# Optimization experiments

Hardware: AMD Instinct MI355X
Metric: run time of the kernel (lower is better)

## Reference

```python
import jax, jax.numpy as jnp
import numpy as np

N_NODES = 10000
N_EDGES = 80000
IN_DIM = 1024
HID = 4096
OUT = 256


def sage_conv(x, src, dst, W_l, b_l, W_r, num_nodes):
    # mean aggregation of source-node features onto target nodes
    msg = x[src]                                            # [E, D] gather
    agg = jax.ops.segment_sum(msg, dst, num_segments=num_nodes)   # [N, D]
    cnt = jax.ops.segment_sum(jnp.ones((src.shape[0],), x.dtype), dst,
                              num_segments=num_nodes)       # [N]
    mean = agg / jnp.clip(cnt, 1.0)[:, None]                # isolated nodes -> 0
    # lin_l(mean) + lin_r(x); lin_r has no bias in PyG SAGEConv
    return mean @ W_l.T + b_l + x @ W_r.T


def setup_inputs() -> dict:
    key = jax.random.key(0)
    ks = jax.random.split(key, 6)
    x = jax.random.normal(ks[0], (N_NODES, IN_DIM), dtype=jnp.float32)
    edge_index = jax.random.randint(ks[1], (2, N_EDGES), 0, N_NODES, dtype=jnp.int32)
    s1 = 1.0 / np.sqrt(IN_DIM)
    s2 = 1.0 / np.sqrt(HID)
    W1_l = jax.random.normal(ks[2], (HID, IN_DIM), dtype=jnp.float32) * s1
    b1_l = jnp.zeros((HID,), jnp.float32)
    W1_r = jax.random.normal(ks[3], (HID, IN_DIM), dtype=jnp.float32) * s1
    W2_l = jax.random.normal(ks[4], (OUT, HID), dtype=jnp.float32) * s2
    b2_l = jnp.zeros((OUT,), jnp.float32)
    W2_r = jax.random.normal(ks[5], (OUT, HID), dtype=jnp.float32) * s2
    return {"x": x, "edge_index": edge_index, "W1_l": W1_l, "b1_l": b1_l,
            "W1_r": W1_r, "W2_l": W2_l, "b2_l": b2_l, "W2_r": W2_r}


def reference(x, edge_index, W1_l, b1_l, W1_r, W2_l, b2_l, W2_r):
    src, dst = edge_index[0], edge_index[1]
    h = sage_conv(x, src, dst, W1_l, b1_l, W1_r, N_NODES)   # [N, 4096]
    h = jax.nn.relu(h)
    # dropout is identity in eval mode
    out = sage_conv(h, src, dst, W2_l, b2_l, W2_r, N_NODES)  # [N, 256]
    return jax.nn.log_softmax(out, axis=1)
```

## Files before the change

### kernel.cpp

```cpp
#include <hip/hip_runtime.h>
#include <cstdint>
#include <cstddef>

#define DEVINL __device__ __forceinline__

typedef __bf16 bf16x8 __attribute__((ext_vector_type(8)));
typedef float f32x4 __attribute__((ext_vector_type(4)));

static constexpr int NN = 10000;
static constexpr int NE = 80000;
static constexpr int IN_DIM = 1024;
static constexpr int HID = 4096;
static constexpr int OUTD = 256;
static constexpr int M_PAD = 10112;

DEVINL unsigned short f2bf(float f) {
  unsigned int u = __builtin_bit_cast(unsigned int, f);
  u += 0x7fffu + ((u >> 16) & 1u);
  return (unsigned short)(u >> 16);
}
DEVINL float bf2f(unsigned short h) {
  unsigned int u = ((unsigned int)h) << 16;
  return __builtin_bit_cast(float, u);
}

DEVINL void ld_lds16(const void* g, void* l) {
  __builtin_amdgcn_global_load_lds(
      (const __attribute__((address_space(1))) unsigned int*)g,
      (__attribute__((address_space(3))) unsigned int*)l, 16, 0, 0);
}

static constexpr int PREP_B1 = 8192;
static constexpr int PREP_B2 = PREP_B1 + 2048;
static constexpr int PREP_B3 = PREP_B2 + 10000;
static constexpr int PREP_NB = PREP_B3 + 313;

__global__ __launch_bounds__(256) void prep_kernel(
    const float* __restrict__ W1l, const float* __restrict__ W1r,
    const float* __restrict__ W2l, const float* __restrict__ W2r,
    const float* __restrict__ x, const int* __restrict__ dst,
    unsigned short* __restrict__ w1cat, unsigned short* __restrict__ w2cat,
    unsigned short* __restrict__ x_bf, int* __restrict__ deg) {
  int b = blockIdx.x;
  int t = threadIdx.x;
  if (b < PREP_B1) {
    int g = b * 256 + t;
    int n = g >> 9;
    int kg = g & 511;
    const float* s = (kg < 256) ? (W1l + (size_t)n * 1024 + kg * 4)
                                : (W1r + (size_t)n * 1024 + (kg - 256) * 4);
    float4 v = *(const float4*)s;
    ushort4 p = {f2bf(v.x), f2bf(v.y), f2bf(v.z), f2bf(v.w)};
    ((ushort4*)w1cat)[g] = p;
  } else if (b < PREP_B2) {
    int g = (b - PREP_B1) * 256 + t;
    int n = g >> 10;
    int kg = g & 1023;
    const float* s = (n < 256) ? (W2l + (size_t)n * 4096 + kg * 4)
                               : (W2r + (size_t)(n - 256) * 4096 + kg * 4);
    float4 v = *(const float4*)s;
    ushort4 p = {f2bf(v.x), f2bf(v.y), f2bf(v.z), f2bf(v.w)};
    ((ushort4*)w2cat)[g] = p;
  } else if (b < PREP_B3) {
    int g = (b - PREP_B2) * 256 + t;
    int i = g >> 8;
    int kg = g & 255;
    float4 v = ((const float4*)(x + (size_t)i * IN_DIM))[kg];
    ushort4 p = {f2bf(v.x), f2bf(v.y), f2bf(v.z), f2bf(v.w)};
    ((ushort4*)(x_bf + (size_t)i * IN_DIM))[kg] = p;
  } else {
    int e = (b - PREP_B3) * 256 + t;
    if (e < NE) atomicAdd(&deg[dst[e]], 1);
  }
}

__global__ __launch_bounds__(256) void scan_kernel(const int* __restrict__ deg,
                                                   int* __restrict__ offs) {
  __shared__ int part[256];
  constexpr int NPT = 40;
  int t = threadIdx.x;
  int base = t * NPT;
  int s = 0;
  for (int j = 0; j < NPT; ++j) {
    int n = base + j;
    s += (n < NN) ? deg[n] : 0;
  }
  part[t] = s;
  __syncthreads();
  for (int o = 1; o < 256; o <<= 1) {
    int v = (t >= o) ? part[t - o] : 0;
    __syncthreads();
    part[t] += v;
    __syncthreads();
  }
  int pre = (t > 0) ? part[t - 1] : 0;
  for (int j = 0; j < NPT; ++j) {
    int n = base + j;
    if (n < NN) {
      offs[n] = pre;
      pre += deg[n];
    }
  }
  if (t == 255) offs[NN] = part[255];
}

__global__ void bin_kernel(const int* __restrict__ src, const int* __restrict__ dst,
                           const int* __restrict__ offs, int* __restrict__ fill,
                           int* __restrict__ csr) {
  int e = blockIdx.x * 256 + threadIdx.x;
  if (e < NE) {
    int d = dst[e];
    int p = atomicAdd(&fill[d], 1);
    csr[offs[d] + p] = src[e];
  }
}

__global__ __launch_bounds__(256) void gather1_kernel(const unsigned short* __restrict__ x_bf,
                                                      const int* __restrict__ offs,
                                                      const int* __restrict__ csr,
                                                      unsigned short* __restrict__ A1) {
  int i = blockIdx.x;
  int t = threadIdx.x;
  int beg = offs[i], end = offs[i + 1];
  float4 acc = {0.f, 0.f, 0.f, 0.f};
  for (int j = beg; j < end; ++j) {
    int s = __builtin_amdgcn_readfirstlane(csr[j]);
    ushort4 u = ((const ushort4*)(x_bf + (size_t)s * IN_DIM))[t];
    acc.x += bf2f(u.x); acc.y += bf2f(u.y); acc.z += bf2f(u.z); acc.w += bf2f(u.w);
  }
  float inv = 1.0f / (float)max(end - beg, 1);
  ushort4 ub = ((const ushort4*)(x_bf + (size_t)i * IN_DIM))[t];
  ushort4 pa = {f2bf(acc.x * inv), f2bf(acc.y * inv), f2bf(acc.z * inv), f2bf(acc.w * inv)};
  unsigned short* row = A1 + (size_t)i * 2048;
  ((ushort4*)row)[t] = pa;
  ((ushort4*)(row + 1024))[t] = ub;
}

template <int BM, int K, int N, int NUMM, int NUMN, int GM, int EPI>
__global__ __launch_bounds__(256) void gemm_kernel(const unsigned short* __restrict__ A,
                                                   const unsigned short* __restrict__ Bt,
                                                   const float* __restrict__ bias,
                                                   void* __restrict__ C0out,
                                                   void* __restrict__ C1out) {
  constexpr int BN = 128;
  constexpr int MI = BM / 32;
  constexpr int NI = 4;
  constexpr int SA = BM / 64;
  constexpr int SB = BN / 64;
  __shared__ unsigned short Asm[BM * 32];
  __shared__ unsigned short Bsm[BN * 32];

  constexpr int NPG = GM * NUMN;
  const int pid = blockIdx.x;
  const int gid = pid / NPG;
  const int first_m = gid * GM;
  const int sz = (NUMM - first_m < GM) ? (NUMM - first_m) : GM;
  const int local = pid % NPG;
  const int pm = first_m + local % sz;
  const int pn = local / sz;

  const int tid = threadIdx.x;
  const int lane = tid & 63;
  const int wave = tid >> 6;
  const int quad = lane >> 4;
  const int l16 = lane & 15;
  const int wm = (wave & 1) * (BM / 2);
  const int wn = (wave >> 1) * 64;
  const long tm0 = (long)pm * BM;
  const long tn0 = (long)pn * BN;

  f32x4 acc[MI][NI];
#pragma unroll
  for (int i = 0; i < MI; ++i)
#pragma unroll
    for (int j = 0; j < NI; ++j) acc[i][j] = (f32x4){0.f, 0.f, 0.f, 0.f};

  const unsigned short* aSrc[SA];
  unsigned short* aDst[SA];
  const unsigned short* bSrc[SB];
  unsigned short* bDst[SB];
#pragma unroll
  for (int s = 0; s < SA; ++s) {
    int c = s * 256 + wave * 64 + lane;
    int r = c >> 2;
    int g = (c & 3) ^ ((r >> 1) & 3);
    aSrc[s] = A + (size_t)(tm0 + r) * K + g * 8;
    aDst[s] = Asm + s * 2048 + wave * 512;
  }
#pragma unroll
  for (int s = 0; s < SB; ++s) {
    int c = s * 256 + wave * 64 + lane;
    int r = c >> 2;
    int g = (c & 3) ^ ((r >> 1) & 3);
    bSrc[s] = Bt + (size_t)(tn0 + r) * K + g * 8;
    bDst[s] = Bsm + s * 2048 + wave * 512;
  }

  const int srd = quad ^ ((l16 >> 1) & 3);

  for (int k0 = 0; k0 < K; k0 += 32) {
#pragma unroll
    for (int s = 0; s < SA; ++s) ld_lds16(aSrc[s] + k0, aDst[s]);
#pragma unroll
    for (int s = 0; s < SB; ++s) ld_lds16(bSrc[s] + k0, bDst[s]);
    __syncthreads();

    bf16x8 af[MI], bv[NI];
#pragma unroll
    for (int i = 0; i < MI; ++i) {
      int ra = wm + i * 16 + l16;
      af[i] = *(const bf16x8*)(Asm + ra * 32 + srd * 8);
    }
#pragma unroll
    for (int j = 0; j < NI; ++j) {
      int rb = wn + j * 16 + l16;
      bv[j] = *(const bf16x8*)(Bsm + rb * 32 + srd * 8);
    }
#pragma unroll
    for (int i = 0; i < MI; ++i)
#pragma unroll
      for (int j = 0; j < NI; ++j)
        acc[i][j] = __builtin_amdgcn_mfma_f32_16x16x32_bf16(af[i], bv[j], acc[i][j], 0, 0, 0);
    __syncthreads();
  }

  if (EPI == 1) {
    unsigned short* C = (unsigned short*)C0out;
#pragma unroll
    for (int i = 0; i < MI; ++i) {
      long m0 = tm0 + wm + i * 16 + quad * 4;
#pragma unroll
      for (int j = 0; j < NI; ++j) {
        int n = (int)tn0 + wn + j * 16 + l16;
        float bvs = bias[n];
#pragma unroll
        for (int r = 0; r < 4; ++r) {
          float v = acc[i][j][r] + bvs;
          v = fmaxf(v, 0.0f);
          C[(size_t)(m0 + r) * N + n] = f2bf(v);
        }
      }
    }
  } else {
    unsigned short* PL = (unsigned short*)C0out;
    float* PR = (float*)C1out;
#pragma unroll
    for (int i = 0; i < MI; ++i) {
      long m0 = tm0 + wm + i * 16 + quad * 4;
#pragma unroll
      for (int j = 0; j < NI; ++j) {
        int n = (int)tn0 + wn + j * 16 + l16;
        if (n < 256) {
#pragma unroll
          for (int r = 0; r < 4; ++r) PL[(size_t)(m0 + r) * 256 + n] = f2bf(acc[i][j][r]);
        } else {
#pragma unroll
          for (int r = 0; r < 4; ++r) PR[(size_t)(m0 + r) * 256 + (n - 256)] = acc[i][j][r];
        }
      }
    }
  }
}

__global__ __launch_bounds__(128) void gather2_final_kernel(const unsigned short* __restrict__ pl,
                                                            const float* __restrict__ pr,
                                                            const int* __restrict__ offs,
                                                            const int* __restrict__ csr,
                                                            const float* __restrict__ b2,
                                                            float* __restrict__ out) {
  int i = blockIdx.x;
  int t = threadIdx.x;
  int beg = offs[i], end = offs[i + 1];
  float a0 = 0.f, a1 = 0.f;
  for (int j = beg; j < end; ++j) {
    int s = __builtin_amdgcn_readfirstlane(csr[j]);
    unsigned int u = ((const unsigned int*)(pl + (size_t)s * 256))[t];
    a0 += bf2f((unsigned short)(u & 0xffffu));
    a1 += bf2f((unsigned short)(u >> 16));
  }
  float inv = 1.0f / (float)max(end - beg, 1);
  float2 bv = ((const float2*)b2)[t];
  float2 pv = ((const float2*)(pr + (size_t)i * 256))[t];
  float v0 = a0 * inv + bv.x + pv.x;
  float v1 = a1 * inv + bv.y + pv.y;

  __shared__ float sm[2], ss[2];
  int w = t >> 6;
  float m = fmaxf(v0, v1);
#pragma unroll
  for (int o = 32; o > 0; o >>= 1) m = fmaxf(m, __shfl_xor(m, o, 64));
  if ((t & 63) == 0) sm[w] = m;
  __syncthreads();
  m = fmaxf(sm[0], sm[1]);

  float s = __expf(v0 - m) + __expf(v1 - m);
#pragma unroll
  for (int o = 32; o > 0; o >>= 1) s += __shfl_xor(s, o, 64);
  if ((t & 63) == 0) ss[w] = s;
  __syncthreads();
  float ls = logf(ss[0] + ss[1]);

  float2 o2 = {v0 - m - ls, v1 - m - ls};
  ((float2*)(out + (size_t)i * OUTD))[t] = o2;
}

static constexpr size_t OFF_A1 = 0;
static constexpr size_t OFF_W1 = OFF_A1 + (size_t)M_PAD * 2048 * 2;
static constexpr size_t OFF_HB = OFF_W1 + (size_t)HID * 2048 * 2;
static constexpr size_t OFF_W2 = OFF_HB + (size_t)M_PAD * HID * 2;
static constexpr size_t OFF_XBF = OFF_W2 - (size_t)NN * IN_DIM * 2;
static constexpr size_t OFF_DEG = OFF_W2 + (size_t)512 * HID * 2;
static constexpr size_t OFF_OFFS = OFF_DEG + (size_t)NN * 4;
static constexpr size_t OFF_FILL = OFF_OFFS + (size_t)(NN + 4) * 4;
static constexpr size_t OFF_CSR = OFF_FILL + (size_t)NN * 4;
static constexpr size_t OFF_PL = OFF_A1;
static constexpr size_t OFF_PR = OFF_PL + (size_t)M_PAD * 256 * 2;

extern "C" void kernel_launch(void* const* d_in, const int* in_sizes, int n_in,
                              void* d_out, int out_size, void* d_ws, size_t ws_size,
                              hipStream_t stream) {
  const float* x = (const float*)d_in[0];
  const int* ei = (const int*)d_in[1];
  const int* src = ei;
  const int* dst = ei + NE;
  const float* W1_l = (const float*)d_in[2];
  const float* b1_l = (const float*)d_in[3];
  const float* W1_r = (const float*)d_in[4];
  const float* W2_l = (const float*)d_in[5];
  const float* b2_l = (const float*)d_in[6];
  const float* W2_r = (const float*)d_in[7];
  float* out = (float*)d_out;

  char* ws = (char*)d_ws;
  unsigned short* A1 = (unsigned short*)(ws + OFF_A1);
  unsigned short* w1cat = (unsigned short*)(ws + OFF_W1);
  unsigned short* h_b = (unsigned short*)(ws + OFF_HB);
  unsigned short* x_bf = (unsigned short*)(ws + OFF_XBF);
  unsigned short* w2cat = (unsigned short*)(ws + OFF_W2);
  int* deg = (int*)(ws + OFF_DEG);
  int* offs = (int*)(ws + OFF_OFFS);
  int* fill = (int*)(ws + OFF_FILL);
  int* csr = (int*)(ws + OFF_CSR);
  unsigned short* pl = (unsigned short*)(ws + OFF_PL);
  float* pr = (float*)(ws + OFF_PR);

  hipMemsetAsync(deg, 0, (size_t)NN * 4, stream);
  hipMemsetAsync(fill, 0, (size_t)NN * 4, stream);
  hipMemsetAsync(A1 + (size_t)NN * 2048, 0, (size_t)(M_PAD - NN) * 2048 * 2, stream);

  prep_kernel<<<PREP_NB, 256, 0, stream>>>(W1_l, W1_r, W2_l, W2_r, x, dst,
                                           w1cat, w2cat, x_bf, deg);
  scan_kernel<<<1, 256, 0, stream>>>(deg, offs);
  bin_kernel<<<(NE + 255) / 256, 256, 0, stream>>>(src, dst, offs, fill, csr);

  gather1_kernel<<<NN, 256, 0, stream>>>(x_bf, offs, csr, A1);

  gemm_kernel<128, 2048, 4096, 79, 32, 32, 1>
      <<<79 * 32, 256, 0, stream>>>(A1, w1cat, b1_l, h_b, nullptr);
  gemm_kernel<64, 4096, 512, 158, 4, 64, 2>
      <<<158 * 4, 256, 0, stream>>>(h_b, w2cat, nullptr, pl, pr);

  gather2_final_kernel<<<NN, 128, 0, stream>>>(pl, pr, offs, csr, b2_l, out);
}
```

Before: 483.9 us.

## Double GEMM K-tile to 64 and fold CSR fill counter into scan

```diff
diff --git a/kernel.cpp b/kernel.cpp
--- a/kernel.cpp
+++ b/kernel.cpp
@@ -75,7 +75,8 @@
 }
 
 __global__ __launch_bounds__(256) void scan_kernel(const int* __restrict__ deg,
-                                                   int* __restrict__ offs) {
+                                                   int* __restrict__ offs,
+                                                   int* __restrict__ cur) {
   __shared__ int part[256];
   constexpr int NPT = 40;
   int t = threadIdx.x;
@@ -98,6 +99,7 @@
     int n = base + j;
     if (n < NN) {
       offs[n] = pre;
+      cur[n] = pre;
       pre += deg[n];
     }
   }
@@ -105,13 +107,11 @@
 }
 
 __global__ void bin_kernel(const int* __restrict__ src, const int* __restrict__ dst,
-                           const int* __restrict__ offs, int* __restrict__ fill,
-                           int* __restrict__ csr) {
+                           int* __restrict__ cur, int* __restrict__ csr) {
   int e = blockIdx.x * 256 + threadIdx.x;
   if (e < NE) {
-    int d = dst[e];
-    int p = atomicAdd(&fill[d], 1);
-    csr[offs[d] + p] = src[e];
+    int p = atomicAdd(&cur[dst[e]], 1);
+    csr[p] = src[e];
   }
 }
 
@@ -145,10 +145,10 @@
   constexpr int BN = 128;
   constexpr int MI = BM / 32;
   constexpr int NI = 4;
-  constexpr int SA = BM / 64;
-  constexpr int SB = BN / 64;
-  __shared__ unsigned short Asm[BM * 32];
-  __shared__ unsigned short Bsm[BN * 32];
+  constexpr int SA = BM / 32;
+  constexpr int SB = BN / 32;
+  __shared__ unsigned short Asm[BM * 64];
+  __shared__ unsigned short Bsm[BN * 64];
 
   constexpr int NPG = GM * NUMN;
   const int pid = blockIdx.x;
@@ -182,45 +182,49 @@
 #pragma unroll
   for (int s = 0; s < SA; ++s) {
     int c = s * 256 + wave * 64 + lane;
-    int r = c >> 2;
-    int g = (c & 3) ^ ((r >> 1) & 3);
+    int r = c >> 3;
+    int g = (c & 7) ^ (r & 7);
     aSrc[s] = A + (size_t)(tm0 + r) * K + g * 8;
     aDst[s] = Asm + s * 2048 + wave * 512;
   }
 #pragma unroll
   for (int s = 0; s < SB; ++s) {
     int c = s * 256 + wave * 64 + lane;
-    int r = c >> 2;
-    int g = (c & 3) ^ ((r >> 1) & 3);
+    int r = c >> 3;
+    int g = (c & 7) ^ (r & 7);
     bSrc[s] = Bt + (size_t)(tn0 + r) * K + g * 8;
     bDst[s] = Bsm + s * 2048 + wave * 512;
   }
 
-  const int srd = quad ^ ((l16 >> 1) & 3);
-
-  for (int k0 = 0; k0 < K; k0 += 32) {
+  const int l7 = l16 & 7;
+
+  for (int k0 = 0; k0 < K; k0 += 64) {
 #pragma unroll
     for (int s = 0; s < SA; ++s) ld_lds16(aSrc[s] + k0, aDst[s]);
 #pragma unroll
     for (int s = 0; s < SB; ++s) ld_lds16(bSrc[s] + k0, bDst[s]);
     __syncthreads();
 
-    bf16x8 af[MI], bv[NI];
-#pragma unroll
-    for (int i = 0; i < MI; ++i) {
-      int ra = wm + i * 16 + l16;
-      af[i] = *(const bf16x8*)(Asm + ra * 32 + srd * 8);
+#pragma unroll
+    for (int kk = 0; kk < 2; ++kk) {
+      const int p = (kk * 4 + quad) ^ l7;
+      bf16x8 af[MI], bv[NI];
+#pragma unroll
+      for (int i = 0; i < MI; ++i) {
+        int ra = wm + i * 16 + l16;
+        af[i] = *(const bf16x8*)(Asm + ra * 64 + p * 8);
+      }
+#pragma unroll
+      for (int j = 0; j < NI; ++j) {
+        int rb = wn + j * 16 + l16;
+        bv[j] = *(const bf16x8*)(Bsm + rb * 64 + p * 8);
+      }
+#pragma unroll
+      for (int i = 0; i < MI; ++i)
+#pragma unroll
+        for (int j = 0; j < NI; ++j)
+          acc[i][j] = __builtin_amdgcn_mfma_f32_16x16x32_bf16(af[i], bv[j], acc[i][j], 0, 0, 0);
     }
-#pragma unroll
-    for (int j = 0; j < NI; ++j) {
-      int rb = wn + j * 16 + l16;
-      bv[j] = *(const bf16x8*)(Bsm + rb * 32 + srd * 8);
-    }
-#pragma unroll
-    for (int i = 0; i < MI; ++i)
-#pragma unroll
-      for (int j = 0; j < NI; ++j)
-        acc[i][j] = __builtin_amdgcn_mfma_f32_16x16x32_bf16(af[i], bv[j], acc[i][j], 0, 0, 0);
     __syncthreads();
   }
 
@@ -311,8 +315,8 @@
 static constexpr size_t OFF_XBF = OFF_W2 - (size_t)NN * IN_DIM * 2;
 static constexpr size_t OFF_DEG = OFF_W2 + (size_t)512 * HID * 2;
 static constexpr size_t OFF_OFFS = OFF_DEG + (size_t)NN * 4;
-static constexpr size_t OFF_FILL = OFF_OFFS + (size_t)(NN + 4) * 4;
-static constexpr size_t OFF_CSR = OFF_FILL + (size_t)NN * 4;
+static constexpr size_t OFF_CUR = OFF_OFFS + (size_t)(NN + 4) * 4;
+static constexpr size_t OFF_CSR = OFF_CUR + (size_t)NN * 4;
 static constexpr size_t OFF_PL = OFF_A1;
 static constexpr size_t OFF_PR = OFF_PL + (size_t)M_PAD * 256 * 2;
 
@@ -339,19 +343,18 @@
   unsigned short* w2cat = (unsigned short*)(ws + OFF_W2);
   int* deg = (int*)(ws + OFF_DEG);
   int* offs = (int*)(ws + OFF_OFFS);
-  int* fill = (int*)(ws + OFF_FILL);
+  int* cur = (int*)(ws + OFF_CUR);
   int* csr = (int*)(ws + OFF_CSR);
   unsigned short* pl = (unsigned short*)(ws + OFF_PL);
   float* pr = (float*)(ws + OFF_PR);
 
   hipMemsetAsync(deg, 0, (size_t)NN * 4, stream);
-  hipMemsetAsync(fill, 0, (size_t)NN * 4, stream);
   hipMemsetAsync(A1 + (size_t)NN * 2048, 0, (size_t)(M_PAD - NN) * 2048 * 2, stream);
 
   prep_kernel<<<PREP_NB, 256, 0, stream>>>(W1_l, W1_r, W2_l, W2_r, x, dst,
                                            w1cat, w2cat, x_bf, deg);
-  scan_kernel<<<1, 256, 0, stream>>>(deg, offs);
-  bin_kernel<<<(NE + 255) / 256, 256, 0, stream>>>(src, dst, offs, fill, csr);
+  scan_kernel<<<1, 256, 0, stream>>>(deg, offs, cur);
+  bin_kernel<<<(NE + 255) / 256, 256, 0, stream>>>(src, dst, cur, csr);
 
   gather1_kernel<<<NN, 256, 0, stream>>>(x_bf, offs, csr, A1);
 
```

Measured after the change: 446.6 us. 1.08x faster.
